# Kernel optimization log

Measured on AMD Instinct MI355X. Metric: run time of the kernel, lower is better.

Reference implementation:

```python
import jax
import jax.numpy as jnp
from jax import lax
import numpy as np

N_PRE = 1024
N_POST = 2048
SEQ_LEN = 4096
DECAY = 0.9   # leak factor per timestep
V_TH = 1.0    # firing threshold


def setup_inputs() -> dict:
    key = jax.random.key(0)
    k1, k2 = jax.random.split(key)
    stim = (jax.random.uniform(k1, (N_PRE, SEQ_LEN), dtype=jnp.float32) < 0.1).astype(jnp.float32)  # sparse input spikes
    weights = jax.random.normal(k2, (N_POST, N_PRE), dtype=jnp.float32) * 0.05
    return {"stim": stim, "weights": weights}


def reference(stim, weights):
    # Synaptic currents for all timesteps at once: cal_post_input(stim[:, i]) == weights @ stim[:, i]
    currents = jnp.einsum("np,pt->nt", weights, stim)  # [n_post, T]

    def lif_step(v, i_t):
        # leaky integrate
        v = v * DECAY + i_t
        # fire
        s = (v >= V_TH).astype(v.dtype)
        # reset to 0 where spiked
        v_next = jnp.where(s > 0, jnp.zeros_like(v), v)
        return v_next, (s, v_next)

    v0 = jnp.zeros((N_POST,), dtype=stim.dtype)
    _, (spikes_t, v_t) = lax.scan(lif_step, v0, currents.T)  # scanned over T
    # transpose back to [n_post, T] to match spike_times / v buffers
    return spikes_t.T, v_t.T
```

## Files before the change

### kernel.cpp

```cpp
#include <hip/hip_runtime.h>

#define N_PRE 1024
#define N_POST 2048
#define SEQ_LEN 4096

#define KSPLIT 512

__device__ __forceinline__ float opaque(float x) {
  asm volatile("" : "+v"(x));
  return x;
}

__device__ __forceinline__ float load_dyn(const void* p, size_t idx, bool isbf) {
  if (isbf) {
    const unsigned short b = ((const unsigned short*)p)[idx];
    return __uint_as_float(((unsigned int)b) << 16);
  }
  return ((const float*)p)[idx];
}

__device__ __forceinline__ int sniff_flags(const void* W, const void* S, int tid,
                                           int* flags_sh) {
  if (tid < 64) {
    const unsigned short* uw = (const unsigned short*)W;
    const float f = fabsf(__uint_as_float(((unsigned int)uw[tid * 2]) << 16));
    const bool big = !(f < 64.f);
    const unsigned long long wb = __ballot(big);
    const unsigned short* us = (const unsigned short*)S;
    int hit = 0;
    for (int j = 0; j < 64; ++j) hit |= (us[tid * 128 + 2 * j] == 0x3F80u) ? 1 : 0;
    const unsigned long long sb = __ballot(hit != 0);
    if (tid == 0) *flags_sh = ((wb == 0ull) ? 1 : 0) | ((sb != 0ull) ? 2 : 0);
  }
  __syncthreads();
  return *flags_sh;
}

__global__ __launch_bounds__(64) void snn_mask_build(const void* __restrict__ W,
                                                     const void* __restrict__ S,
                                                     unsigned char* __restrict__ MT) {
  __shared__ int flags_sh;
  const int tid = threadIdx.x;
  const int fl = sniff_flags(W, S, tid, &flags_sh);
  const bool s_bf = (fl & 2) != 0;
  const int tb = blockIdx.x;
  unsigned wrd[4] = {0u, 0u, 0u, 0u};
#pragma unroll
  for (int kk = 0; kk < 16; ++kk) {
    const int k = tid * 16 + kk;
    unsigned byte = 0;
    if (s_bf) {
      const unsigned short* Sb = (const unsigned short*)S;
      const uint4 u = *(const uint4*)&Sb[(size_t)k * SEQ_LEN + tb * 8];
      byte |= (((u.x & 0x7FFFu) != 0u) ? 1u : 0u) << 0;
      byte |= (((u.x & 0x7FFF0000u) != 0u) ? 1u : 0u) << 1;
      byte |= (((u.y & 0x7FFFu) != 0u) ? 1u : 0u) << 2;
      byte |= (((u.y & 0x7FFF0000u) != 0u) ? 1u : 0u) << 3;
      byte |= (((u.z & 0x7FFFu) != 0u) ? 1u : 0u) << 4;
      byte |= (((u.z & 0x7FFF0000u) != 0u) ? 1u : 0u) << 5;
      byte |= (((u.w & 0x7FFFu) != 0u) ? 1u : 0u) << 6;
      byte |= (((u.w & 0x7FFF0000u) != 0u) ? 1u : 0u) << 7;
    } else {
      const float* Sf = (const float*)S;
      const size_t base = (size_t)k * SEQ_LEN + tb * 8;
      const float4 f0 = *(const float4*)&Sf[base];
      const float4 f1 = *(const float4*)&Sf[base + 4];
      byte |= ((f0.x != 0.0f) ? 1u : 0u) << 0;
      byte |= ((f0.y != 0.0f) ? 1u : 0u) << 1;
      byte |= ((f0.z != 0.0f) ? 1u : 0u) << 2;
      byte |= ((f0.w != 0.0f) ? 1u : 0u) << 3;
      byte |= ((f1.x != 0.0f) ? 1u : 0u) << 4;
      byte |= ((f1.y != 0.0f) ? 1u : 0u) << 5;
      byte |= ((f1.z != 0.0f) ? 1u : 0u) << 6;
      byte |= ((f1.w != 0.0f) ? 1u : 0u) << 7;
    }
    wrd[kk >> 2] |= byte << ((kk & 3) * 8);
  }
  *(uint4*)&MT[(size_t)tb * N_PRE + tid * 16] =
      make_uint4(wrd[0], wrd[1], wrd[2], wrd[3]);
}

__global__ __launch_bounds__(256, 2) void snn_gemm_v5(const void* __restrict__ W,
                                                      const void* __restrict__ S,
                                                      const unsigned char* __restrict__ MT,
                                                      float* __restrict__ C,
                                                      int t0, int ct) {
  __shared__ float As[16][132];
  __shared__ int flags_sh;
  const int tid = threadIdx.x;
  const int fl = sniff_flags(W, S, tid, &flags_sh);
  const bool w_bf = (fl & 1) != 0;

  const int tx = tid & 15;
  const int ty = tid >> 4;
  const int m0 = blockIdx.y * 128;
  const int nl0 = blockIdx.x * 128;
  const int kbeg = (int)blockIdx.z * KSPLIT;
  const size_t mrow = (size_t)((t0 + nl0 + tx * 8) >> 3) * N_PRE;

  float acc[8][8] = {{0.f}};

  for (int k0 = kbeg; k0 < kbeg + KSPLIT; k0 += 16) {
    if (!w_bf) {
      const float* Wf = (const float*)W;
      const int row = tid >> 2;
      const int c4 = (tid & 3) * 4;
#pragma unroll
      for (int h = 0; h < 2; ++h) {
        const int m = row + 64 * h;
        const float4 va = *(const float4*)&Wf[(size_t)(m0 + m) * N_PRE + k0 + c4];
        As[c4 + 0][m] = va.x; As[c4 + 1][m] = va.y;
        As[c4 + 2][m] = va.z; As[c4 + 3][m] = va.w;
      }
    } else {
#pragma unroll
      for (int e = 0; e < 8; ++e) {
        const int idx = tid * 8 + e;
        const int m = idx >> 4, c = idx & 15;
        As[c][m] = load_dyn(W, (size_t)(m0 + m) * N_PRE + k0 + c, true);
      }
    }
    const uint4 mk = *(const uint4*)&MT[mrow + k0];
    const unsigned mw0 = mk.x, mw1 = mk.y, mw2 = mk.z, mw3 = mk.w;
    __syncthreads();
#pragma unroll
    for (int k = 0; k < 16; ++k) {
      float a[8];
      *(float4*)&a[0] = *(const float4*)&As[k][ty * 8];
      *(float4*)&a[4] = *(const float4*)&As[k][ty * 8 + 4];
      const unsigned mwsel = (k < 4) ? mw0 : (k < 8) ? mw1 : (k < 12) ? mw2 : mw3;
      const unsigned mb = (mwsel >> ((k & 3) * 8)) & 0xFFu;
      float b[8];
#pragma unroll
      for (int j = 0; j < 8; ++j)
        b[j] = __int_as_float(0x3F800000 & (((int)(mb << (31 - j))) >> 31));
#pragma unroll
      for (int i = 0; i < 8; ++i)
#pragma unroll
        for (int j = 0; j < 8; ++j)
          acc[i][j] += a[i] * b[j];
    }
    __syncthreads();
  }

  float* Cseg = C + (size_t)blockIdx.z * N_POST * (size_t)ct;
#pragma unroll
  for (int i = 0; i < 8; ++i) {
    float* dst = &Cseg[(size_t)(m0 + ty * 8 + i) * ct + nl0 + tx * 8];
    *(float4*)&dst[0] = make_float4(acc[i][0], acc[i][1], acc[i][2], acc[i][3]);
    *(float4*)&dst[4] = make_float4(acc[i][4], acc[i][5], acc[i][6], acc[i][7]);
  }
}

#define SCAN_R 8
#define SCAN_T 64
#define SCAN_P 68
__global__ __launch_bounds__(64) void snn_scan_v3(const float* __restrict__ C,
                                                  float* __restrict__ spk,
                                                  float* __restrict__ vout,
                                                  float* __restrict__ v_carry,
                                                  int t0, int ct, int first) {
  __shared__ float c_t[2][SCAN_R][SCAN_P];
  const int l = threadIdx.x;
  const int n0 = blockIdx.x * SCAN_R;
  const float* C1 = C + (size_t)N_POST * (size_t)ct;

  float v = 0.0f;
  if (l < SCAN_R && !first) v = v_carry[n0 + l];

  const int r0 = l >> 4;
  const int c4 = (l & 15) * 4;
  const int ntiles = ct / SCAN_T;

#pragma unroll
  for (int h = 0; h < 2; ++h) {
    const int r = r0 + 4 * h;
    const size_t g = (size_t)(n0 + r) * ct + c4;
    const float4 a = *(const float4*)&C[g];
    const float4 b = *(const float4*)&C1[g];
    *(float4*)&c_t[0][r][c4] =
        make_float4(a.x + b.x, a.y + b.y, a.z + b.z, a.w + b.w);
  }

  int buf = 0;
  for (int it = 0; it < ntiles; ++it) {
    float4 pa[2], pb[2];
    const bool pf = (it + 1 < ntiles);
    if (pf) {
#pragma unroll
      for (int h = 0; h < 2; ++h) {
        const int r = r0 + 4 * h;
        const size_t g = (size_t)(n0 + r) * ct + (size_t)(it + 1) * SCAN_T + c4;
        pa[h] = *(const float4*)&C[g];
        pb[h] = *(const float4*)&C1[g];
      }
    }
    if (l < SCAN_R) {
      const size_t gout = (size_t)(n0 + l) * SEQ_LEN + t0 + (size_t)it * SCAN_T;
#pragma unroll
      for (int g = 0; g < SCAN_T / 16; ++g) {
        float c[16];
        *(float4*)&c[0] = *(const float4*)&c_t[buf][l][g * 16];
        *(float4*)&c[4] = *(const float4*)&c_t[buf][l][g * 16 + 4];
        *(float4*)&c[8] = *(const float4*)&c_t[buf][l][g * 16 + 8];
        *(float4*)&c[12] = *(const float4*)&c_t[buf][l][g * 16 + 12];
        float s[16], vv[16];
#pragma unroll
        for (int k = 0; k < 16; ++k) {
          const float leak = opaque(v * 0.9f);
          v = leak + c[k];
          const bool fired = (v >= 1.0f);
          s[k] = fired ? 1.0f : 0.0f;
          v = fired ? 0.0f : v;
          vv[k] = v;
        }
#pragma unroll
        for (int q = 0; q < 4; ++q) {
          *(float4*)&spk[gout + g * 16 + q * 4] =
              make_float4(s[q * 4], s[q * 4 + 1], s[q * 4 + 2], s[q * 4 + 3]);
          *(float4*)&vout[gout + g * 16 + q * 4] =
              make_float4(vv[q * 4], vv[q * 4 + 1], vv[q * 4 + 2], vv[q * 4 + 3]);
        }
      }
    }
    if (pf) {
#pragma unroll
      for (int h = 0; h < 2; ++h) {
        const int r = r0 + 4 * h;
        *(float4*)&c_t[buf ^ 1][r][c4] =
            make_float4(pa[h].x + pb[h].x, pa[h].y + pb[h].y, pa[h].z + pb[h].z,
                        pa[h].w + pb[h].w);
      }
    }
    buf ^= 1;
  }
  if (l < SCAN_R) v_carry[n0 + l] = v;
}

__global__ __launch_bounds__(256) void snn_fused_blis(const void* __restrict__ W,
                                                      const void* __restrict__ S,
                                                      float* __restrict__ spk,
                                                      float* __restrict__ vout) {
  __shared__ float As[16][68];
  __shared__ float Bs[16][68];
  __shared__ float Ct[64][65];
  __shared__ float vsh[64];
  __shared__ int flags_sh;
  const int tid = threadIdx.x;
  const int fl = sniff_flags(W, S, tid, &flags_sh);
  const bool w_bf = (fl & 1) != 0;
  const bool s_bf = (fl & 2) != 0;

  const int tx = tid & 15;
  const int ty = tid >> 4;
  const int m0 = blockIdx.x * 64;
  if (tid < 64) vsh[tid] = 0.0f;

  for (int t0 = 0; t0 < SEQ_LEN; t0 += 64) {
    float acc0[4][4] = {{0.f}};
    float acc1[4][4] = {{0.f}};
    int k0 = 0;
#define FUSED_SEGMENT(ACC, KEND)                                                 \
    for (; k0 < (KEND); k0 += 16) {                                              \
      {                                                                          \
        const int r = tid >> 4, c = tid & 15;                                    \
        _Pragma("unroll") for (int j = 0; j < 4; ++j)                            \
            As[c][r + 16 * j] =                                                  \
                load_dyn(W, (size_t)(m0 + r + 16 * j) * N_PRE + k0 + c, w_bf);   \
      }                                                                          \
      {                                                                          \
        const int r = tid >> 6, c = tid & 63;                                    \
        _Pragma("unroll") for (int j = 0; j < 4; ++j)                            \
            Bs[r + 4 * j][c] =                                                   \
                load_dyn(S, (size_t)(k0 + r + 4 * j) * SEQ_LEN + t0 + c, s_bf);  \
      }                                                                          \
      __syncthreads();                                                           \
      _Pragma("unroll") for (int k = 0; k < 16; ++k) {                           \
        _Pragma("unroll") for (int i = 0; i < 4; ++i)                            \
            _Pragma("unroll") for (int j = 0; j < 4; ++j)                        \
                ACC[i][j] += As[k][ty * 4 + i] * Bs[k][tx * 4 + j];              \
      }                                                                          \
      __syncthreads();                                                           \
    }

    FUSED_SEGMENT(acc0, KSPLIT)
    FUSED_SEGMENT(acc1, N_PRE)
#undef FUSED_SEGMENT

#pragma unroll
    for (int i = 0; i < 4; ++i)
#pragma unroll
      for (int j = 0; j < 4; ++j) Ct[ty * 4 + i][tx * 4 + j] = acc0[i][j] + acc1[i][j];
    __syncthreads();
    if (tid < 64) {
      float v = vsh[tid];
#pragma unroll
      for (int k = 0; k < 64; ++k) {
        const float leak = opaque(v * 0.9f);
        v = leak + Ct[tid][k];
        const bool fired = (v >= 1.0f);
        const size_t g = (size_t)(m0 + tid) * SEQ_LEN + t0 + k;
        spk[g] = fired ? 1.0f : 0.0f;
        v = fired ? 0.0f : v;
        vout[g] = v;
      }
      vsh[tid] = v;
    }
    __syncthreads();
  }
}

extern "C" void kernel_launch(void* const* d_in, const int* in_sizes, int n_in,
                              void* d_out, int out_size, void* d_ws, size_t ws_size,
                              hipStream_t stream) {
  const void* stim = d_in[0];
  const void* weights = d_in[1];
  if (n_in >= 2 && in_sizes[0] == N_POST * N_PRE && in_sizes[1] == N_PRE * SEQ_LEN) {
    weights = d_in[0];
    stim = d_in[1];
  }

  float* spk = (float*)d_out;
  float* vout = spk + (size_t)N_POST * SEQ_LEN;

  const size_t carry_bytes = (size_t)N_POST * sizeof(float);
  const size_t mask_sz = (size_t)(SEQ_LEN / 8) * N_PRE;
  float* v_carry = nullptr;
  unsigned char* MT = nullptr;
  size_t avail = 0;
  if (ws_size > carry_bytes + mask_sz + 1024) {
    const size_t coff = (ws_size - carry_bytes) & ~(size_t)15;
    v_carry = (float*)((char*)d_ws + coff);
    const size_t moff = (coff - mask_sz) & ~(size_t)15;
    MT = (unsigned char*)d_ws + moff;
    avail = moff;
  }
  int chunkT = (int)((avail / ((size_t)N_POST * sizeof(float) * 2)) / 128 * 128);
  if (chunkT > SEQ_LEN) chunkT = SEQ_LEN;
  if (chunkT >= 128) {
    int p = 128;
    while (p * 2 <= chunkT && p < SEQ_LEN) p *= 2;
    chunkT = p;
  }

  if (chunkT >= 128) {
    float* cur = (float*)d_ws;
    snn_mask_build<<<dim3(SEQ_LEN / 8), dim3(64), 0, stream>>>(weights, stim, MT);
    for (int t0 = 0; t0 < SEQ_LEN; t0 += chunkT) {
      const int ct = (SEQ_LEN - t0 < chunkT) ? (SEQ_LEN - t0) : chunkT;
      snn_gemm_v5<<<dim3(ct / 128, N_POST / 128, 2), dim3(256), 0, stream>>>(
          weights, stim, MT, cur, t0, ct);
      snn_scan_v3<<<dim3(N_POST / SCAN_R), dim3(64), 0, stream>>>(
          cur, spk, vout, v_carry, t0, ct, t0 == 0);
    }
  } else {
    snn_fused_blis<<<dim3(N_POST / 64), dim3(256), 0, stream>>>(weights, stim, spk, vout);
  }
}
```

Before: 422.2 us.

## Replace dense masked GEMM with sparse gather over active-input index lists

Builds a transposed weight matrix and per-timestep lists of active presynaptic indices, then computes currents by summing only the weight rows for spiking inputs instead of a dense 128x128-tiled GEMM. This exploits the roughly 10% input spike density to cut the arithmetic and weight traffic. The scan is reworked to hold a 64-neuron by 64-step tile in registers, reading C laid out time-major, and staging outputs through shared memory for stores. The change adds preprocessing kernels and a larger workspace, and the gather loads depend on spike density and may serialize unevenly across timesteps.

```diff
diff --git a/kernel.cpp b/kernel.cpp
--- a/kernel.cpp
+++ b/kernel.cpp
@@ -34,6 +34,53 @@
   }
   __syncthreads();
   return *flags_sh;
+}
+
+__global__ __launch_bounds__(256) void snn_wt_build(const void* __restrict__ W,
+                                                    const void* __restrict__ S,
+                                                    float* __restrict__ WT) {
+  __shared__ float tile[64][65];
+  __shared__ int flags_sh;
+  const int tid = threadIdx.x;
+  const int fl = sniff_flags(W, S, tid, &flags_sh);
+  const bool w_bf = (fl & 1) != 0;
+  const int k0 = blockIdx.x * 64;
+  const int nn0 = blockIdx.y * 64;
+  {
+    const int r = tid >> 2;
+    const int cq = tid & 3;
+    if (!w_bf) {
+      const float* Wf = (const float*)W;
+#pragma unroll
+      for (int p = 0; p < 4; ++p) {
+        const int c = cq * 16 + p * 4;
+        const float4 va = *(const float4*)&Wf[(size_t)(nn0 + r) * N_PRE + k0 + c];
+        tile[c + 0][r] = va.x; tile[c + 1][r] = va.y;
+        tile[c + 2][r] = va.z; tile[c + 3][r] = va.w;
+      }
+    } else {
+#pragma unroll
+      for (int p = 0; p < 4; ++p)
+#pragma unroll
+        for (int j = 0; j < 4; ++j) {
+          const int c = cq * 16 + p * 4 + j;
+          tile[c][r] = load_dyn(W, (size_t)(nn0 + r) * N_PRE + k0 + c, true);
+        }
+    }
+  }
+  __syncthreads();
+  {
+    const int kr = tid >> 2;
+    const int nq = tid & 3;
+#pragma unroll
+    for (int p = 0; p < 4; ++p) {
+      const int c = nq * 16 + p * 4;
+      float4 o;
+      o.x = tile[kr][c + 0]; o.y = tile[kr][c + 1];
+      o.z = tile[kr][c + 2]; o.w = tile[kr][c + 3];
+      *(float4*)&WT[(size_t)(k0 + kr) * N_POST + nn0 + c] = o;
+    }
+  }
 }
 
 __global__ __launch_bounds__(64) void snn_mask_build(const void* __restrict__ W,
@@ -80,161 +127,130 @@
       make_uint4(wrd[0], wrd[1], wrd[2], wrd[3]);
 }
 
-__global__ __launch_bounds__(256, 2) void snn_gemm_v5(const void* __restrict__ W,
-                                                      const void* __restrict__ S,
-                                                      const unsigned char* __restrict__ MT,
-                                                      float* __restrict__ C,
-                                                      int t0, int ct) {
-  __shared__ float As[16][132];
-  __shared__ int flags_sh;
-  const int tid = threadIdx.x;
-  const int fl = sniff_flags(W, S, tid, &flags_sh);
-  const bool w_bf = (fl & 1) != 0;
-
-  const int tx = tid & 15;
-  const int ty = tid >> 4;
-  const int m0 = blockIdx.y * 128;
-  const int nl0 = blockIdx.x * 128;
-  const int kbeg = (int)blockIdx.z * KSPLIT;
-  const size_t mrow = (size_t)((t0 + nl0 + tx * 8) >> 3) * N_PRE;
-
-  float acc[8][8] = {{0.f}};
-
-  for (int k0 = kbeg; k0 < kbeg + KSPLIT; k0 += 16) {
-    if (!w_bf) {
-      const float* Wf = (const float*)W;
-      const int row = tid >> 2;
-      const int c4 = (tid & 3) * 4;
-#pragma unroll
-      for (int h = 0; h < 2; ++h) {
-        const int m = row + 64 * h;
-        const float4 va = *(const float4*)&Wf[(size_t)(m0 + m) * N_PRE + k0 + c4];
-        As[c4 + 0][m] = va.x; As[c4 + 1][m] = va.y;
-        As[c4 + 2][m] = va.z; As[c4 + 3][m] = va.w;
-      }
-    } else {
-#pragma unroll
-      for (int e = 0; e < 8; ++e) {
-        const int idx = tid * 8 + e;
-        const int m = idx >> 4, c = idx & 15;
-        As[c][m] = load_dyn(W, (size_t)(m0 + m) * N_PRE + k0 + c, true);
-      }
-    }
-    const uint4 mk = *(const uint4*)&MT[mrow + k0];
-    const unsigned mw0 = mk.x, mw1 = mk.y, mw2 = mk.z, mw3 = mk.w;
-    __syncthreads();
-#pragma unroll
-    for (int k = 0; k < 16; ++k) {
-      float a[8];
-      *(float4*)&a[0] = *(const float4*)&As[k][ty * 8];
-      *(float4*)&a[4] = *(const float4*)&As[k][ty * 8 + 4];
-      const unsigned mwsel = (k < 4) ? mw0 : (k < 8) ? mw1 : (k < 12) ? mw2 : mw3;
-      const unsigned mb = (mwsel >> ((k & 3) * 8)) & 0xFFu;
-      float b[8];
-#pragma unroll
-      for (int j = 0; j < 8; ++j)
-        b[j] = __int_as_float(0x3F800000 & (((int)(mb << (31 - j))) >> 31));
-#pragma unroll
-      for (int i = 0; i < 8; ++i)
-#pragma unroll
-        for (int j = 0; j < 8; ++j)
-          acc[i][j] += a[i] * b[j];
-    }
-    __syncthreads();
-  }
-
-  float* Cseg = C + (size_t)blockIdx.z * N_POST * (size_t)ct;
-#pragma unroll
-  for (int i = 0; i < 8; ++i) {
-    float* dst = &Cseg[(size_t)(m0 + ty * 8 + i) * ct + nl0 + tx * 8];
-    *(float4*)&dst[0] = make_float4(acc[i][0], acc[i][1], acc[i][2], acc[i][3]);
-    *(float4*)&dst[4] = make_float4(acc[i][4], acc[i][5], acc[i][6], acc[i][7]);
-  }
-}
-
-#define SCAN_R 8
-#define SCAN_T 64
-#define SCAN_P 68
-__global__ __launch_bounds__(64) void snn_scan_v3(const float* __restrict__ C,
+__global__ __launch_bounds__(64) void snn_list_build(const unsigned char* __restrict__ MT,
+                                                     unsigned short* __restrict__ lists,
+                                                     int* __restrict__ lens,
+                                                     int* __restrict__ splits) {
+  const int t = blockIdx.x;
+  const int l = threadIdx.x;
+  const unsigned char* Mrow = MT + (size_t)(t >> 3) * N_PRE;
+  const int bit = t & 7;
+  unsigned short* Lp = lists + (size_t)t * N_PRE;
+  int base = 0;
+  int split = 0;
+#pragma unroll
+  for (int c = 0; c < 16; ++c) {
+    const int k = c * 64 + l;
+    const int b = (Mrow[k] >> bit) & 1;
+    const unsigned long long m = __ballot(b != 0);
+    const int pre = __popcll(m & ((1ull << l) - 1ull));
+    if (b) Lp[base + pre] = (unsigned short)k;
+    base += __popcll(m);
+    if (c == 7) split = base;
+  }
+  if (l == 0) {
+    lens[t] = base;
+    splits[t] = split;
+  }
+}
+
+__global__ __launch_bounds__(256) void snn_gemm_sp(const float* __restrict__ WT,
+                                                   const unsigned short* __restrict__ lists,
+                                                   const int* __restrict__ lens,
+                                                   const int* __restrict__ splits,
+                                                   float* __restrict__ C,
+                                                   int t0, int ct) {
+  const int tl = blockIdx.x;
+  const int tg = t0 + tl;
+  const int n = (int)blockIdx.y * 1024 + (int)threadIdx.x * 4;
+  const unsigned short* __restrict__ L = lists + (size_t)tg * N_PRE;
+  const int len = lens[tg];
+  const int sp = splits[tg];
+  float lo0 = 0.f, lo1 = 0.f, lo2 = 0.f, lo3 = 0.f;
+  float hi0 = 0.f, hi1 = 0.f, hi2 = 0.f, hi3 = 0.f;
+  int i = 0;
+  for (; i < sp; ++i) {
+    const int k = L[i];
+    const float4 w = *(const float4*)&WT[((size_t)k << 11) + n];
+    lo0 += w.x; lo1 += w.y; lo2 += w.z; lo3 += w.w;
+  }
+  for (; i < len; ++i) {
+    const int k = L[i];
+    const float4 w = *(const float4*)&WT[((size_t)k << 11) + n];
+    hi0 += w.x; hi1 += w.y; hi2 += w.z; hi3 += w.w;
+  }
+  *(float4*)&C[(size_t)tl * N_POST + n] =
+      make_float4(lo0 + hi0, lo1 + hi1, lo2 + hi2, lo3 + hi3);
+}
+
+__global__ __launch_bounds__(64) void snn_scan_v4(const float* __restrict__ C,
                                                   float* __restrict__ spk,
                                                   float* __restrict__ vout,
                                                   float* __restrict__ v_carry,
                                                   int t0, int ct, int first) {
-  __shared__ float c_t[2][SCAN_R][SCAN_P];
+  __shared__ float sb[2][64][65];
+  __shared__ float vb[2][64][65];
   const int l = threadIdx.x;
-  const int n0 = blockIdx.x * SCAN_R;
-  const float* C1 = C + (size_t)N_POST * (size_t)ct;
-
+  const int n0 = blockIdx.x * 64;
   float v = 0.0f;
-  if (l < SCAN_R && !first) v = v_carry[n0 + l];
-
-  const int r0 = l >> 4;
-  const int c4 = (l & 15) * 4;
-  const int ntiles = ct / SCAN_T;
-
-#pragma unroll
-  for (int h = 0; h < 2; ++h) {
-    const int r = r0 + 4 * h;
-    const size_t g = (size_t)(n0 + r) * ct + c4;
-    const float4 a = *(const float4*)&C[g];
-    const float4 b = *(const float4*)&C1[g];
-    *(float4*)&c_t[0][r][c4] =
-        make_float4(a.x + b.x, a.y + b.y, a.z + b.z, a.w + b.w);
-  }
-
-  int buf = 0;
-  for (int it = 0; it < ntiles; ++it) {
-    float4 pa[2], pb[2];
-    const bool pf = (it + 1 < ntiles);
-    if (pf) {
-#pragma unroll
-      for (int h = 0; h < 2; ++h) {
-        const int r = r0 + 4 * h;
-        const size_t g = (size_t)(n0 + r) * ct + (size_t)(it + 1) * SCAN_T + c4;
-        pa[h] = *(const float4*)&C[g];
-        pb[h] = *(const float4*)&C1[g];
-      }
-    }
-    if (l < SCAN_R) {
-      const size_t gout = (size_t)(n0 + l) * SEQ_LEN + t0 + (size_t)it * SCAN_T;
-#pragma unroll
-      for (int g = 0; g < SCAN_T / 16; ++g) {
-        float c[16];
-        *(float4*)&c[0] = *(const float4*)&c_t[buf][l][g * 16];
-        *(float4*)&c[4] = *(const float4*)&c_t[buf][l][g * 16 + 4];
-        *(float4*)&c[8] = *(const float4*)&c_t[buf][l][g * 16 + 8];
-        *(float4*)&c[12] = *(const float4*)&c_t[buf][l][g * 16 + 12];
-        float s[16], vv[16];
-#pragma unroll
-        for (int k = 0; k < 16; ++k) {
-          const float leak = opaque(v * 0.9f);
-          v = leak + c[k];
-          const bool fired = (v >= 1.0f);
-          s[k] = fired ? 1.0f : 0.0f;
-          v = fired ? 0.0f : v;
-          vv[k] = v;
+  if (!first) v = v_carry[n0 + l];
+  const int ntiles = ct / 64;
+
+  float ccur[64], cnxt[64];
+#pragma unroll
+  for (int j = 0; j < 64; ++j) ccur[j] = C[(size_t)j * N_POST + n0 + l];
+
+  for (int tile = 0; tile < ntiles; ++tile) {
+    __syncthreads();
+    const int buf = tile & 1;
+    const bool havePrev = (tile > 0);
+    const bool haveNext = (tile + 1 < ntiles);
+#pragma unroll
+    for (int g = 0; g < 4; ++g) {
+      if (haveNext) {
+#pragma unroll
+        for (int j = 0; j < 16; ++j)
+          cnxt[g * 16 + j] =
+              C[(size_t)((tile + 1) * 64 + g * 16 + j) * N_POST + n0 + l];
+      }
+#pragma unroll
+      for (int j = 0; j < 16; ++j) {
+        const float c = ccur[g * 16 + j];
+        const float leak = opaque(v * 0.9f);
+        v = leak + c;
+        const bool fired = (v >= 1.0f);
+        const float s = fired ? 1.0f : 0.0f;
+        v = fired ? 0.0f : v;
+        sb[buf][g * 16 + j][l] = s;
+        vb[buf][g * 16 + j][l] = v;
+      }
+      if (havePrev) {
+        const int pb = buf ^ 1;
+        const size_t gt = (size_t)t0 + (size_t)(tile - 1) * 64 + l;
+#pragma unroll
+        for (int r = 0; r < 16; ++r) {
+          const int row = g * 16 + r;
+          const size_t go = (size_t)(n0 + row) * SEQ_LEN + gt;
+          spk[go] = sb[pb][l][row];
+          vout[go] = vb[pb][l][row];
         }
-#pragma unroll
-        for (int q = 0; q < 4; ++q) {
-          *(float4*)&spk[gout + g * 16 + q * 4] =
-              make_float4(s[q * 4], s[q * 4 + 1], s[q * 4 + 2], s[q * 4 + 3]);
-          *(float4*)&vout[gout + g * 16 + q * 4] =
-              make_float4(vv[q * 4], vv[q * 4 + 1], vv[q * 4 + 2], vv[q * 4 + 3]);
-        }
-      }
-    }
-    if (pf) {
-#pragma unroll
-      for (int h = 0; h < 2; ++h) {
-        const int r = r0 + 4 * h;
-        *(float4*)&c_t[buf ^ 1][r][c4] =
-            make_float4(pa[h].x + pb[h].x, pa[h].y + pb[h].y, pa[h].z + pb[h].z,
-                        pa[h].w + pb[h].w);
-      }
-    }
-    buf ^= 1;
-  }
-  if (l < SCAN_R) v_carry[n0 + l] = v;
+      }
+    }
+#pragma unroll
+    for (int j = 0; j < 64; ++j) ccur[j] = cnxt[j];
+  }
+  __syncthreads();
+  {
+    const int pb = (ntiles - 1) & 1;
+    const size_t gt = (size_t)t0 + (size_t)(ntiles - 1) * 64 + l;
+#pragma unroll
+    for (int row = 0; row < 64; ++row) {
+      const size_t go = (size_t)(n0 + row) * SEQ_LEN + gt;
+      spk[go] = sb[pb][l][row];
+      vout[go] = vb[pb][l][row];
+    }
+  }
+  v_carry[n0 + l] = v;
 }
 
 __global__ __launch_bounds__(256) void snn_fused_blis(const void* __restrict__ W,
@@ -323,35 +339,34 @@
   float* spk = (float*)d_out;
   float* vout = spk + (size_t)N_POST * SEQ_LEN;
 
-  const size_t carry_bytes = (size_t)N_POST * sizeof(float);
-  const size_t mask_sz = (size_t)(SEQ_LEN / 8) * N_PRE;
-  float* v_carry = nullptr;
-  unsigned char* MT = nullptr;
-  size_t avail = 0;
-  if (ws_size > carry_bytes + mask_sz + 1024) {
-    const size_t coff = (ws_size - carry_bytes) & ~(size_t)15;
-    v_carry = (float*)((char*)d_ws + coff);
-    const size_t moff = (coff - mask_sz) & ~(size_t)15;
-    MT = (unsigned char*)d_ws + moff;
-    avail = moff;
-  }
-  int chunkT = (int)((avail / ((size_t)N_POST * sizeof(float) * 2)) / 128 * 128);
+  char* p = (char*)d_ws;
+  float* WT = (float*)p;                 p += (size_t)N_PRE * N_POST * 4;
+  unsigned char* MT = (unsigned char*)p; p += (size_t)(SEQ_LEN / 8) * N_PRE;
+  unsigned short* lists = (unsigned short*)p; p += (size_t)SEQ_LEN * N_PRE * 2;
+  int* lens = (int*)p;                   p += (size_t)SEQ_LEN * 4;
+  int* splits = (int*)p;                 p += (size_t)SEQ_LEN * 4;
+  float* v_carry = (float*)p;            p += (size_t)N_POST * 4;
+  float* C = (float*)p;
+  const size_t used = (size_t)(p - (char*)d_ws);
+  const size_t remain = (ws_size > used) ? (ws_size - used) : 0;
+
+  int chunkT = (int)((remain / ((size_t)N_POST * sizeof(float))) / 64 * 64);
   if (chunkT > SEQ_LEN) chunkT = SEQ_LEN;
-  if (chunkT >= 128) {
-    int p = 128;
-    while (p * 2 <= chunkT && p < SEQ_LEN) p *= 2;
-    chunkT = p;
-  }
-
-  if (chunkT >= 128) {
-    float* cur = (float*)d_ws;
+  if (chunkT >= 64) {
+    int pw = 64;
+    while (pw * 2 <= chunkT && pw < SEQ_LEN) pw *= 2;
+    chunkT = pw;
+  }
+
+  if (chunkT >= 64) {
+    snn_wt_build<<<dim3(N_PRE / 64, N_POST / 64), dim3(256), 0, stream>>>(weights, stim, WT);
     snn_mask_build<<<dim3(SEQ_LEN / 8), dim3(64), 0, stream>>>(weights, stim, MT);
+    snn_list_build<<<dim3(SEQ_LEN), dim3(64), 0, stream>>>(MT, lists, lens, splits);
     for (int t0 = 0; t0 < SEQ_LEN; t0 += chunkT) {
       const int ct = (SEQ_LEN - t0 < chunkT) ? (SEQ_LEN - t0) : chunkT;
-      snn_gemm_v5<<<dim3(ct / 128, N_POST / 128, 2), dim3(256), 0, stream>>>(
-          weights, stim, MT, cur, t0, ct);
-      snn_scan_v3<<<dim3(N_POST / SCAN_R), dim3(64), 0, stream>>>(
-          cur, spk, vout, v_carry, t0, ct, t0 == 0);
+      snn_gemm_sp<<<dim3(ct, 2), dim3(256), 0, stream>>>(WT, lists, lens, splits, C, t0, ct);
+      snn_scan_v4<<<dim3(N_POST / 64), dim3(64), 0, stream>>>(C, spk, vout, v_carry,
+                                                              t0, ct, t0 == 0);
     }
   } else {
     snn_fused_blis<<<dim3(N_POST / 64), dim3(256), 0, stream>>>(weights, stim, spk, vout);
```

Result: slower. 564.3 us (+33.7%).
